# Optimization experiments

Hardware: AMD Instinct MI355X
Metric: run time of the kernel (lower is better)

## Reference

```python
import jax, jax.numpy as jnp
import numpy as np

N = 50000
E = 800000
IN_DIM = 128
HID = 128
HEADS = 8
OUT_DIM = 64
LRELU_SLOPE = 0.2


def setup_inputs() -> dict:
    key = jax.random.key(0)
    ks = jax.random.split(key, 10)
    x = jax.random.normal(ks[0], (N, IN_DIM), dtype=jnp.float32)
    edge_index = jax.random.randint(ks[1], (2, E), 0, N, dtype=jnp.int64)
    c1 = HID // HEADS  # 16
    W1 = jax.random.normal(ks[2], (IN_DIM, HID), dtype=jnp.float32) * (1.0 / np.sqrt(IN_DIM))
    as1 = jax.random.normal(ks[3], (HEADS, c1), dtype=jnp.float32) * 0.1
    ad1 = jax.random.normal(ks[4], (HEADS, c1), dtype=jnp.float32) * 0.1
    b1 = jnp.zeros((HID,), dtype=jnp.float32)
    W2 = jax.random.normal(ks[5], (HID, OUT_DIM), dtype=jnp.float32) * (1.0 / np.sqrt(HID))
    as2 = jax.random.normal(ks[6], (1, OUT_DIM), dtype=jnp.float32) * 0.1
    ad2 = jax.random.normal(ks[7], (1, OUT_DIM), dtype=jnp.float32) * 0.1
    b2 = jnp.zeros((OUT_DIM,), dtype=jnp.float32)
    return {"x": x, "edge_index": edge_index, "W1": W1, "as1": as1, "ad1": ad1,
            "b1": b1, "W2": W2, "as2": as2, "ad2": ad2, "b2": b2}


def gat_conv(x, src, dst, W, a_src, a_dst, b, heads, ch, concat):
    n = x.shape[0]
    h = (x @ W).reshape(n, heads, ch)               # [N,H,C]
    alpha_s = jnp.sum(h * a_src, axis=-1)           # [N,H]
    alpha_d = jnp.sum(h * a_dst, axis=-1)           # [N,H]
    e = jax.nn.leaky_relu(alpha_s[src] + alpha_d[dst], LRELU_SLOPE)  # [E,H]
    m = jax.ops.segment_max(e, dst, num_segments=n)  # per-dst max (self-loops guarantee nonempty)
    e = jnp.exp(e - m[dst])
    denom = jax.ops.segment_sum(e, dst, num_segments=n)
    alpha = e / (denom[dst] + 1e-16)                # [E,H]
    msg = h[src] * alpha[:, :, None]                # [E,H,C]
    out = jax.ops.segment_sum(msg, dst, num_segments=n)  # [N,H,C]
    out = out.reshape(n, heads * ch) if concat else out.mean(axis=1)
    return out + b


def reference(x, edge_index, W1, as1, ad1, b1, W2, as2, ad2, b2):
    n = x.shape[0]
    loops = jnp.arange(n, dtype=edge_index.dtype)
    src = jnp.concatenate([edge_index[0], loops])   # PyG GATConv adds self-loops
    dst = jnp.concatenate([edge_index[1], loops])
    # layer 1: GATBlock (dropout is identity at eval), heads=8, concat, ELU
    h = gat_conv(x, src, dst, W1, as1, ad1, b1, HEADS, HID // HEADS, True)
    h = jax.nn.elu(h)
    # final conv: heads=1, concat=False
    out = gat_conv(h, src, dst, W2, as2, ad2, b2, 1, OUT_DIM, False)
    return jax.nn.log_softmax(out, axis=1)
```

## Files before the change

### kernel.cpp

```cpp
#include <hip/hip_runtime.h>
#include <hip/hip_bf16.h>
#include <math.h>

#define IN_DIM 128
#define HID 128
#define HEADS 8
#define OUT_DIM 64
#define SLOPE 0.2f
#define BSHIFT 7
#define BCAP 4096
#define BCAPSHIFT 12
#define EPT 8

typedef short bf16x8 __attribute__((ext_vector_type(8)));
typedef float f32x4 __attribute__((ext_vector_type(4)));

__device__ __forceinline__ float lrelu(float x) { return fmaxf(x, SLOPE * x); }
__device__ __forceinline__ float bf2f(unsigned u) { return __uint_as_float(u << 16); }
__device__ __forceinline__ unsigned short f2bf(float f) {
    unsigned u = __float_as_uint(f);
    return (unsigned short)((u + 0x7FFF + ((u >> 16) & 1)) >> 16);
}

__global__ __launch_bounds__(256) void setup_kernel(
    const float* __restrict__ W1, const float* __restrict__ W2,
    short* __restrict__ w1t, short* __restrict__ w2t, int* __restrict__ gcursor) {
    int t = threadIdx.x;
    int b = blockIdx.x;
    if (b == 96) {
        for (int i = t; i < 512; i += 256) gcursor[i] = 0;
        return;
    }
    if (b < 64) {
        int id = b * 256 + t;
        int n = id >> 7, k = id & 127;
        w1t[id] = (short)f2bf(W1[k * 128 + n]);
    } else {
        int id = (b - 64) * 256 + t;
        int n = id >> 7, k = id & 127;
        w2t[id] = (short)f2bf(W2[k * 64 + n]);
    }
}

__device__ __forceinline__ void bscatter_body(
    int blk, int* smem, const int* __restrict__ idx,
    int* __restrict__ gcursor, unsigned* __restrict__ bucket_buf,
    int E, int N, int NB) {
    int* hist  = smem;
    int* gbase = smem + 512;
    int* lbase = smem + 1024;
    int* wtot  = smem + 1536;
    int* misc  = smem + 1540;
    unsigned* sent = (unsigned*)(smem + 1552);
    unsigned* spos = (unsigned*)(smem + 3600);
    int t = threadIdx.x;
    for (int i = t; i < 512; i += 256) hist[i] = 0;
    if (t == 0) misc[1] = 0;
    __syncthreads();
    {
        int nz = (idx[2 * t + 1] != 0) + (idx[2 * t + 513] != 0);
        if (nz) atomicAdd(&misc[1], nz);
    }
    __syncthreads();
    int flag = (misc[1] > 16) ? 1 : 0;
    int e0 = blk * (256 * EPT);
    int EN = E + N;
    unsigned ent[EPT];
    int bid[EPT];
    int loc[EPT];
#pragma unroll
    for (int k = 0; k < EPT; k++) {
        int e = e0 + k * 256 + t;
        bid[k] = -1;
        if (e < EN) {
            int src, dst;
            if (e < E) {
                if (flag) { src = idx[e]; dst = idx[E + e]; }
                else      { src = idx[2 * e]; dst = idx[2 * (E + e)]; }
            } else {
                src = dst = e - E;
            }
            int b = dst >> BSHIFT;
            bid[k] = b;
            ent[k] = ((unsigned)(dst & ((1 << BSHIFT) - 1)) << 16) | (unsigned)src;
            loc[k] = atomicAdd(&hist[b], 1);
        }
    }
    __syncthreads();
    int i0 = 2 * t;
    int a = hist[i0], b2 = hist[i0 + 1];
    int ps = a + b2;
    int lane = t & 63, w = t >> 6;
    int incl = ps;
#pragma unroll
    for (int off = 1; off < 64; off <<= 1) {
        int u = __shfl_up(incl, off, 64);
        if (lane >= off) incl += u;
    }
    if (lane == 63) wtot[w] = incl;
    __syncthreads();
    int woff = 0;
    for (int k = 0; k < w; k++) woff += wtot[k];
    int ex0 = woff + incl - ps;
    lbase[i0] = ex0;
    lbase[i0 + 1] = ex0 + a;
    if (t == 255) misc[0] = woff + incl;
    for (int i = t; i < 512; i += 256) {
        int c = hist[i];
        gbase[i] = c ? atomicAdd(&gcursor[i], c) : 0;
    }
    __syncthreads();
#pragma unroll
    for (int k = 0; k < EPT; k++) {
        if (bid[k] >= 0) {
            int p = lbase[bid[k]] + loc[k];
            int pib = gbase[bid[k]] + loc[k];
            sent[p] = ent[k];
            spos[p] = (pib < BCAP) ? (((unsigned)bid[k] << BCAPSHIFT) | (unsigned)pib)
                                   : 0xFFFFFFFFu;
        }
    }
    __syncthreads();
    int tot = misc[0];
    for (int i = t; i < tot; i += 256) {
        unsigned sp = spos[i];
        if (sp != 0xFFFFFFFFu) bucket_buf[sp] = sent[i];
    }
}

__device__ __forceinline__ void gemm1_body(
    int blk, char* smemraw, const float* __restrict__ x, const short* __restrict__ w1t,
    const float* __restrict__ a_s, const float* __restrict__ a_d,
    unsigned short* __restrict__ h1g, float* __restrict__ as_n,
    float* __restrict__ ad_n, int N) {
    short* Wt = (short*)smemraw;
    float* hT = (float*)smemraw;
    int t = threadIdx.x;
    const uint4* src = (const uint4*)w1t;
    for (int id = t; id < 128 * 16; id += 256) {
        int n = id >> 4, kg = id & 15;
        *(uint4*)&Wt[n * 128 + ((kg * 8) ^ ((n & 7) << 3))] = src[id];
    }
    __syncthreads();
    int wv = t >> 6, lane = t & 63;
    int m = lane & 15, q = lane >> 4;
    int row = blk * 64 + wv * 16 + m;
    f32x4 acc[8];
#pragma unroll
    for (int j = 0; j < 8; j++) acc[j] = (f32x4){0.f, 0.f, 0.f, 0.f};
    int msw = (m & 7) << 3;
#pragma unroll
    for (int k0 = 0; k0 < 128; k0 += 32) {
        bf16x8 a = {0, 0, 0, 0, 0, 0, 0, 0};
        if (row < N) {
            const float* xp = &x[(size_t)row * 128 + k0 + q * 8];
            float4 u0 = *(const float4*)xp;
            float4 u1 = *(const float4*)(xp + 4);
            a[0] = (short)f2bf(u0.x); a[1] = (short)f2bf(u0.y);
            a[2] = (short)f2bf(u0.z); a[3] = (short)f2bf(u0.w);
            a[4] = (short)f2bf(u1.x); a[5] = (short)f2bf(u1.y);
            a[6] = (short)f2bf(u1.z); a[7] = (short)f2bf(u1.w);
        }
#pragma unroll
        for (int j = 0; j < 8; j++) {
            bf16x8 b = *(const bf16x8*)&Wt[(j * 16 + m) * 128 + ((k0 + q * 8) ^ msw)];
            acc[j] = __builtin_amdgcn_mfma_f32_16x16x32_bf16(a, b, acc[j], 0, 0, 0);
        }
    }
    __syncthreads();
#pragma unroll
    for (int r = 0; r < 4; r++) {
        int rl = wv * 16 + q * 4 + r;
        int sw = ((rl >> 2) & 1) << 4;
        int rb = rl * 128;
#pragma unroll
        for (int j = 0; j < 8; j++)
            hT[rb + ((j * 16 + m) ^ sw)] = acc[j][r];
    }
    __syncthreads();
    int base = blk * 64;
    for (int id = t; id < 1024; id += 256) {
        int rl = id >> 4, c8 = (id & 15) * 8;
        int rg = base + rl;
        if (rg >= N) continue;
        int sw = ((rl >> 2) & 1) << 4;
        float4 u0 = *(const float4*)&hT[rl * 128 + (c8 ^ sw)];
        float4 u1 = *(const float4*)&hT[rl * 128 + ((c8 + 4) ^ sw)];
        uint4 ow;
        ow.x = (unsigned)f2bf(u0.x) | ((unsigned)f2bf(u0.y) << 16);
        ow.y = (unsigned)f2bf(u0.z) | ((unsigned)f2bf(u0.w) << 16);
        ow.z = (unsigned)f2bf(u1.x) | ((unsigned)f2bf(u1.y) << 16);
        ow.w = (unsigned)f2bf(u1.z) | ((unsigned)f2bf(u1.w) << 16);
        *(uint4*)&h1g[(size_t)rg * 128 + c8] = ow;
    }
    for (int it = t; it < 512; it += 256) {
        int rl = it >> 3, hd = it & 7;
        int rg = base + rl;
        int sw = ((rl >> 2) & 1) << 4;
        const float* ap = a_s + hd * 16;
        const float* dp = a_d + hd * 16;
        float s = 0.f, d = 0.f;
#pragma unroll
        for (int p = 0; p < 4; p++) {
            float4 u = *(const float4*)&hT[rl * 128 + ((hd * 16 + p * 4) ^ sw)];
            s += u.x * ap[p * 4] + u.y * ap[p * 4 + 1] + u.z * ap[p * 4 + 2] + u.w * ap[p * 4 + 3];
            d += u.x * dp[p * 4] + u.y * dp[p * 4 + 1] + u.z * dp[p * 4 + 2] + u.w * dp[p * 4 + 3];
        }
        if (rg < N) {
            as_n[(size_t)base * 8 + it] = s;
            ad_n[(size_t)base * 8 + it] = d;
        }
    }
}

__global__ __launch_bounds__(256) void k1_kernel(
    const int* __restrict__ idx, int* __restrict__ gcursor,
    unsigned* __restrict__ bucket_buf,
    const float* __restrict__ x, const short* __restrict__ w1t,
    const float* __restrict__ a_s, const float* __restrict__ a_d,
    unsigned short* __restrict__ h1g, float* __restrict__ as_n,
    float* __restrict__ ad_n, int E, int N, int NB, int GS) {
    __shared__ long long smem[4096];
    if ((int)blockIdx.x < GS)
        bscatter_body(blockIdx.x, (int*)smem, idx, gcursor, bucket_buf, E, N, NB);
    else
        gemm1_body(blockIdx.x - GS, (char*)smem, x, w1t, a_s, a_d, h1g, as_n, ad_n, N);
}

__device__ __forceinline__ void bsort_body(
    int b, const int* __restrict__ gcursor, const unsigned* __restrict__ bucket_buf,
    int* __restrict__ row_start, int* __restrict__ sorted_src, int N, int NB) {
    __shared__ int cnt[128];
    __shared__ int cur[128];
    __shared__ int red[4];
    __shared__ int s_w0;
    __shared__ int srt[BCAP];
    int t = threadIdx.x;
    if (t < 128) cnt[t] = 0;
    int partial = 0;
    for (int i = t; i < b; i += 256) partial += min(gcursor[i], BCAP);
#pragma unroll
    for (int msk = 32; msk > 0; msk >>= 1) partial += __shfl_xor(partial, msk, 64);
    if ((t & 63) == 0) red[t >> 6] = partial;
    __syncthreads();
    int bbase = red[0] + red[1] + red[2] + red[3];
    int c = min(gcursor[b], BCAP);
    const unsigned* buf = bucket_buf + ((size_t)b << BCAPSHIFT);
    for (int i = t; i < c; i += 256)
        atomicAdd(&cnt[(buf[i] >> 16) & 127], 1);
    __syncthreads();
    int v = (t < 128) ? cnt[t] : 0;
    int lane = t & 63;
    int incl = v;
#pragma unroll
    for (int off = 1; off < 64; off <<= 1) {
        int u = __shfl_up(incl, off, 64);
        if (lane >= off) incl += u;
    }
    if (t == 63) s_w0 = incl;
    __syncthreads();
    if (t < 128) {
        int excl = incl - v + ((t >= 64) ? s_w0 : 0);
        cur[t] = excl;
        int node = (b << BSHIFT) + t;
        if (node <= N) row_start[node] = bbase + excl;
    }
    __syncthreads();
    for (int i = t; i < c; i += 256) {
        unsigned e = buf[i];
        int lp = atomicAdd(&cur[(e >> 16) & 127], 1);
        srt[lp] = (int)(e & 0xFFFFu);
    }
    __syncthreads();
    for (int i = t; i < c; i += 256)
        sorted_src[bbase + i] = srt[i];
}

__global__ __launch_bounds__(256) void k2_kernel(
    const int* __restrict__ gcursor, const unsigned* __restrict__ bucket_buf,
    int* __restrict__ row_start, int* __restrict__ sorted_src,
    int N, int NB, int EN) {
    if (blockIdx.x == 0 && threadIdx.x < 16) sorted_src[EN + threadIdx.x] = 0;
    bsort_body(blockIdx.x, gcursor, bucket_buf, row_start, sorted_src, N, NB);
}

__global__ __launch_bounds__(256) void agg1_kernel(
    const int* __restrict__ row_start, const int* __restrict__ sorted_src,
    const float* __restrict__ as_n, const float* __restrict__ ad_n,
    const unsigned short* __restrict__ h1g, const float* __restrict__ b1,
    unsigned short* __restrict__ h1act, int N) {
    int lane = threadIdx.x & 63;
    int g = lane >> 4, j = lane & 15;
    int node = blockIdx.x * 16 + (threadIdx.x >> 6) * 4 + g;
    if (node >= N) return;
    int e4 = j >> 2;
    int hh = (j & 3) * 2;
    int hd = j >> 1;
    int hsel = hd & 1;
    int wsrc = hd >> 1;
    float2 adp = *(const float2*)&ad_n[(size_t)node * 8 + hh];
    int beg = row_start[node], end = row_start[node + 1];
    float acc[8];
#pragma unroll
    for (int k = 0; k < 8; k++) acc[k] = 0.f;
    float denom = 0.f;
    for (int i = beg; i < end; i += 4) {
        int se = sorted_src[i + e4];
        float2 asp = *(const float2*)&as_n[(size_t)se * 8 + hh];
        float w0 = __expf(lrelu(asp.x + adp.x));
        float w1 = __expf(lrelu(asp.y + adp.y));
        bool val = (i + e4 < end);
        w0 = val ? w0 : 0.f;
        w1 = val ? w1 : 0.f;
#pragma unroll
        for (int e = 0; e < 4; e++) {
            int sl = e * 4 + wsrc;
            int sg = __shfl(se, sl, 16);
            float wa = __shfl(w0, sl, 16);
            float wb = __shfl(w1, sl, 16);
            float wv = hsel ? wb : wa;
            uint4 hv = *(const uint4*)&h1g[(size_t)sg * 128 + j * 8];
            acc[0] += wv * bf2f(hv.x & 0xffffu);
            acc[1] += wv * bf2f(hv.x >> 16);
            acc[2] += wv * bf2f(hv.y & 0xffffu);
            acc[3] += wv * bf2f(hv.y >> 16);
            acc[4] += wv * bf2f(hv.z & 0xffffu);
            acc[5] += wv * bf2f(hv.z >> 16);
            acc[6] += wv * bf2f(hv.w & 0xffffu);
            acc[7] += wv * bf2f(hv.w >> 16);
            denom += wv;
        }
    }
    float inv = 1.f / (denom + 1e-16f);
    int c0 = j * 8;
    unsigned ow[4];
#pragma unroll
    for (int p = 0; p < 4; p++) {
        float v0 = acc[2 * p] * inv + b1[c0 + 2 * p];
        float v1 = acc[2 * p + 1] * inv + b1[c0 + 2 * p + 1];
        v0 = (v0 > 0.f) ? v0 : (__expf(v0) - 1.f);
        v1 = (v1 > 0.f) ? v1 : (__expf(v1) - 1.f);
        ow[p] = (unsigned)f2bf(v0) | ((unsigned)f2bf(v1) << 16);
    }
    *(uint4*)&h1act[(size_t)node * 128 + c0] = make_uint4(ow[0], ow[1], ow[2], ow[3]);
}

__global__ __launch_bounds__(256) void gemm2_kernel(
    const unsigned short* __restrict__ h1act, const short* __restrict__ w2t,
    const float* __restrict__ a_s, const float* __restrict__ a_d,
    unsigned short* __restrict__ h2g, float* __restrict__ as_n,
    float* __restrict__ ad_n, int N) {
    __shared__ short Wt[64 * 136];
    int t = threadIdx.x;
    const uint4* src = (const uint4*)w2t;
    for (int id = t; id < 64 * 16; id += 256) {
        int n = id >> 4, kg = id & 15;
        *(uint4*)&Wt[n * 136 + kg * 8] = src[id];
    }
    __syncthreads();
    int wv = t >> 6, lane = t & 63;
    int m = lane & 15, q = lane >> 4;
    int row = blockIdx.x * 64 + wv * 16 + m;
    f32x4 acc[4];
#pragma unroll
    for (int j = 0; j < 4; j++) acc[j] = (f32x4){0.f, 0.f, 0.f, 0.f};
#pragma unroll
    for (int k0 = 0; k0 < 128; k0 += 32) {
        bf16x8 a = {0, 0, 0, 0, 0, 0, 0, 0};
        if (row < N) a = *(const bf16x8*)&h1act[(size_t)row * 128 + k0 + q * 8];
#pragma unroll
        for (int j = 0; j < 4; j++) {
            bf16x8 b = *(const bf16x8*)&Wt[(j * 16 + m) * 136 + k0 + q * 8];
            acc[j] = __builtin_amdgcn_mfma_f32_16x16x32_bf16(a, b, acc[j], 0, 0, 0);
        }
    }
    float asl[4], adl[4];
#pragma unroll
    for (int j = 0; j < 4; j++) { asl[j] = a_s[j * 16 + m]; adl[j] = a_d[j * 16 + m]; }
    int rbase = blockIdx.x * 64 + wv * 16 + q * 4;
#pragma unroll
    for (int r = 0; r < 4; r++) {
        int rr = rbase + r;
        float s = 0.f, d = 0.f;
#pragma unroll
        for (int j = 0; j < 4; j++) {
            s += acc[j][r] * asl[j];
            d += acc[j][r] * adl[j];
        }
#pragma unroll
        for (int msk = 8; msk > 0; msk >>= 1) {
            s += __shfl_xor(s, msk, 64);
            d += __shfl_xor(d, msk, 64);
        }
        if (rr < N) {
            if (m == 0) { as_n[rr] = s; ad_n[rr] = d; }
#pragma unroll
            for (int j = 0; j < 4; j++)
                h2g[(size_t)rr * 64 + j * 16 + m] = f2bf(acc[j][r]);
        }
    }
}

__global__ __launch_bounds__(256) void agg2_kernel(
    const int* __restrict__ row_start, const int* __restrict__ sorted_src,
    const float* __restrict__ as_n, const float* __restrict__ ad_n,
    const unsigned short* __restrict__ h2g, const float* __restrict__ b2,
    float* __restrict__ out, int N) {
    int lane = threadIdx.x & 63;
    int g = lane >> 4, j = lane & 15;
    int node = blockIdx.x * 16 + (threadIdx.x >> 6) * 4 + g;
    if (node >= N) return;
    int e4 = j >> 2;
    float adv = ad_n[node];
    int beg = row_start[node], end = row_start[node + 1];
    float acc[4];
#pragma unroll
    for (int k = 0; k < 4; k++) acc[k] = 0.f;
    float denom = 0.f;
    for (int i = beg; i < end; i += 4) {
        int se = sorted_src[i + e4];
        float w = __expf(lrelu(as_n[se] + adv));
        w = (i + e4 < end) ? w : 0.f;
#pragma unroll
        for (int e = 0; e < 4; e++) {
            int sg = __shfl(se, e * 4, 16);
            float wvv = __shfl(w, e * 4, 16);
            uint2 hv = *(const uint2*)&h2g[(size_t)sg * 64 + j * 4];
            acc[0] += wvv * bf2f(hv.x & 0xffffu);
            acc[1] += wvv * bf2f(hv.x >> 16);
            acc[2] += wvv * bf2f(hv.y & 0xffffu);
            acc[3] += wvv * bf2f(hv.y >> 16);
            denom += wvv;
        }
    }
    float inv = 1.f / (denom + 1e-16f);
    int c0 = j * 4;
    float v[4];
#pragma unroll
    for (int k = 0; k < 4; k++) v[k] = acc[k] * inv + b2[c0 + k];
    float mx = fmaxf(fmaxf(v[0], v[1]), fmaxf(v[2], v[3]));
#pragma unroll
    for (int msk = 8; msk > 0; msk >>= 1) mx = fmaxf(mx, __shfl_xor(mx, msk, 64));
    float ex = __expf(v[0] - mx) + __expf(v[1] - mx) + __expf(v[2] - mx) + __expf(v[3] - mx);
#pragma unroll
    for (int msk = 8; msk > 0; msk >>= 1) ex += __shfl_xor(ex, msk, 64);
    float lse = mx + __logf(ex);
    *(float4*)&out[(size_t)node * 64 + c0] = make_float4(v[0] - lse, v[1] - lse, v[2] - lse, v[3] - lse);
}

extern "C" void kernel_launch(void* const* d_in, const int* in_sizes, int n_in,
                              void* d_out, int out_size, void* d_ws, size_t ws_size,
                              hipStream_t stream) {
    const float* x   = (const float*)d_in[0];
    const int*   idx = (const int*)d_in[1];
    const float* W1  = (const float*)d_in[2];
    const float* as1 = (const float*)d_in[3];
    const float* ad1 = (const float*)d_in[4];
    const float* b1  = (const float*)d_in[5];
    const float* W2  = (const float*)d_in[6];
    const float* as2 = (const float*)d_in[7];
    const float* ad2 = (const float*)d_in[8];
    const float* b2  = (const float*)d_in[9];
    float* out = (float*)d_out;

    const int N = in_sizes[0] / IN_DIM;
    const int E = in_sizes[1] / 2;
    const int EN = E + N;
    const int NB = (N + (1 << BSHIFT) - 1) >> BSHIFT;
    const int GS = (EN + 256 * EPT - 1) / (256 * EPT);
    const int T1 = (N + 63) / 64;

    unsigned short* h1g   = (unsigned short*)d_ws;
    unsigned short* h1act = h1g + (size_t)N * 128;
    unsigned short* h2g   = h1act + (size_t)N * 128;
    float* as1n = (float*)(h2g + (size_t)N * 64);
    float* ad1n = as1n + (size_t)N * 8;
    float* as2n = ad1n + (size_t)N * 8;
    float* ad2n = as2n + (size_t)N;
    int* row_start  = (int*)(ad2n + (size_t)N);
    int* gcursor    = row_start + N + 1;
    unsigned* bucket_buf = (unsigned*)(gcursor + 512);
    int* sorted_src = (int*)(bucket_buf + ((size_t)NB << BCAPSHIFT));
    short* w1t = (short*)((((uintptr_t)(sorted_src + EN + 16)) + 15) & ~(uintptr_t)15);
    short* w2t = w1t + 128 * 128;
    (void)ws_size; (void)n_in; (void)out_size;

    setup_kernel<<<97, 256, 0, stream>>>(W1, W2, w1t, w2t, gcursor);
    k1_kernel<<<GS + T1, 256, 0, stream>>>(idx, gcursor, bucket_buf,
                                           x, w1t, as1, ad1, h1g, as1n, ad1n, E, N, NB, GS);
    k2_kernel<<<NB, 256, 0, stream>>>(gcursor, bucket_buf, row_start, sorted_src, N, NB, EN);
    agg1_kernel<<<(N + 15) / 16, 256, 0, stream>>>(row_start, sorted_src, as1n, ad1n, h1g, b1, h1act, N);
    gemm2_kernel<<<T1, 256, 0, stream>>>(h1act, w2t, as2, ad2, h2g, as2n, ad2n, N);
    agg2_kernel<<<(N + 15) / 16, 256, 0, stream>>>(row_start, sorted_src, as2n, ad2n, h2g, b2, out, N);
}
```

Before: 187.8 us.

## Fuse layer-1 aggregation with layer-2 GEMM via shared-memory tile

Merges the layer-1 attention aggregation and the layer-2 MFMA projection into one kernel. Each block aggregates 64 nodes, writes the ELU-activated bf16 rows into a swizzled LDS tile, then runs the 64x128x64 MFMA GEMM from LDS. This removes the h1act global write and re-read plus one launch. In exchange, blocks are 4x fewer (64 nodes each, processed serially in 4 passes) and use about 33KB of LDS, which can reduce occupancy and the latency hiding available to the gather-bound aggregation.

```diff
diff --git a/kernel.cpp b/kernel.cpp
--- a/kernel.cpp
+++ b/kernel.cpp
@@ -284,108 +284,112 @@
     bsort_body(blockIdx.x, gcursor, bucket_buf, row_start, sorted_src, N, NB);
 }
 
-__global__ __launch_bounds__(256) void agg1_kernel(
+__global__ __launch_bounds__(256) void mid_kernel(
     const int* __restrict__ row_start, const int* __restrict__ sorted_src,
     const float* __restrict__ as_n, const float* __restrict__ ad_n,
     const unsigned short* __restrict__ h1g, const float* __restrict__ b1,
-    unsigned short* __restrict__ h1act, int N) {
-    int lane = threadIdx.x & 63;
+    const short* __restrict__ w2t, const float* __restrict__ a_s2,
+    const float* __restrict__ a_d2, unsigned short* __restrict__ h2g,
+    float* __restrict__ as2n, float* __restrict__ ad2n, int N) {
+    __shared__ short hA[64 * 128];
+    __shared__ short Wt[64 * 136];
+    int t = threadIdx.x;
+    const uint4* srcw = (const uint4*)w2t;
+    for (int id = t; id < 64 * 16; id += 256) {
+        int n = id >> 4, kg = id & 15;
+        *(uint4*)&Wt[n * 136 + kg * 8] = srcw[id];
+    }
+    int lane = t & 63;
     int g = lane >> 4, j = lane & 15;
-    int node = blockIdx.x * 16 + (threadIdx.x >> 6) * 4 + g;
-    if (node >= N) return;
+    int base = blockIdx.x * 64;
+    int grp16 = (t >> 6) * 4 + g;
     int e4 = j >> 2;
     int hh = (j & 3) * 2;
     int hd = j >> 1;
     int hsel = hd & 1;
     int wsrc = hd >> 1;
-    float2 adp = *(const float2*)&ad_n[(size_t)node * 8 + hh];
-    int beg = row_start[node], end = row_start[node + 1];
-    float acc[8];
-#pragma unroll
-    for (int k = 0; k < 8; k++) acc[k] = 0.f;
-    float denom = 0.f;
-    for (int i = beg; i < end; i += 4) {
-        int se = sorted_src[i + e4];
-        float2 asp = *(const float2*)&as_n[(size_t)se * 8 + hh];
-        float w0 = __expf(lrelu(asp.x + adp.x));
-        float w1 = __expf(lrelu(asp.y + adp.y));
-        bool val = (i + e4 < end);
-        w0 = val ? w0 : 0.f;
-        w1 = val ? w1 : 0.f;
-#pragma unroll
-        for (int e = 0; e < 4; e++) {
-            int sl = e * 4 + wsrc;
-            int sg = __shfl(se, sl, 16);
-            float wa = __shfl(w0, sl, 16);
-            float wb = __shfl(w1, sl, 16);
-            float wv = hsel ? wb : wa;
-            uint4 hv = *(const uint4*)&h1g[(size_t)sg * 128 + j * 8];
-            acc[0] += wv * bf2f(hv.x & 0xffffu);
-            acc[1] += wv * bf2f(hv.x >> 16);
-            acc[2] += wv * bf2f(hv.y & 0xffffu);
-            acc[3] += wv * bf2f(hv.y >> 16);
-            acc[4] += wv * bf2f(hv.z & 0xffffu);
-            acc[5] += wv * bf2f(hv.z >> 16);
-            acc[6] += wv * bf2f(hv.w & 0xffffu);
-            acc[7] += wv * bf2f(hv.w >> 16);
-            denom += wv;
-        }
-    }
-    float inv = 1.f / (denom + 1e-16f);
-    int c0 = j * 8;
-    unsigned ow[4];
-#pragma unroll
-    for (int p = 0; p < 4; p++) {
-        float v0 = acc[2 * p] * inv + b1[c0 + 2 * p];
-        float v1 = acc[2 * p + 1] * inv + b1[c0 + 2 * p + 1];
-        v0 = (v0 > 0.f) ? v0 : (__expf(v0) - 1.f);
-        v1 = (v1 > 0.f) ? v1 : (__expf(v1) - 1.f);
-        ow[p] = (unsigned)f2bf(v0) | ((unsigned)f2bf(v1) << 16);
-    }
-    *(uint4*)&h1act[(size_t)node * 128 + c0] = make_uint4(ow[0], ow[1], ow[2], ow[3]);
-}
-
-__global__ __launch_bounds__(256) void gemm2_kernel(
-    const unsigned short* __restrict__ h1act, const short* __restrict__ w2t,
-    const float* __restrict__ a_s, const float* __restrict__ a_d,
-    unsigned short* __restrict__ h2g, float* __restrict__ as_n,
-    float* __restrict__ ad_n, int N) {
-    __shared__ short Wt[64 * 136];
-    int t = threadIdx.x;
-    const uint4* src = (const uint4*)w2t;
-    for (int id = t; id < 64 * 16; id += 256) {
-        int n = id >> 4, kg = id & 15;
-        *(uint4*)&Wt[n * 136 + kg * 8] = src[id];
-    }
-    __syncthreads();
-    int wv = t >> 6, lane = t & 63;
+    for (int ni = 0; ni < 4; ni++) {
+        int rowl = ni * 16 + grp16;
+        int node = base + rowl;
+        float acc[8];
+#pragma unroll
+        for (int k = 0; k < 8; k++) acc[k] = 0.f;
+        float denom = 0.f;
+        if (node < N) {
+            float2 adp = *(const float2*)&ad_n[(size_t)node * 8 + hh];
+            int beg = row_start[node], end = row_start[node + 1];
+            for (int i = beg; i < end; i += 4) {
+                int se = sorted_src[i + e4];
+                float2 asp = *(const float2*)&as_n[(size_t)se * 8 + hh];
+                float w0 = __expf(lrelu(asp.x + adp.x));
+                float w1 = __expf(lrelu(asp.y + adp.y));
+                bool val = (i + e4 < end);
+                w0 = val ? w0 : 0.f;
+                w1 = val ? w1 : 0.f;
+#pragma unroll
+                for (int e = 0; e < 4; e++) {
+                    int sl = e * 4 + wsrc;
+                    int sg = __shfl(se, sl, 16);
+                    float wa = __shfl(w0, sl, 16);
+                    float wb = __shfl(w1, sl, 16);
+                    float wv = hsel ? wb : wa;
+                    uint4 hv = *(const uint4*)&h1g[(size_t)sg * 128 + j * 8];
+                    acc[0] += wv * bf2f(hv.x & 0xffffu);
+                    acc[1] += wv * bf2f(hv.x >> 16);
+                    acc[2] += wv * bf2f(hv.y & 0xffffu);
+                    acc[3] += wv * bf2f(hv.y >> 16);
+                    acc[4] += wv * bf2f(hv.z & 0xffffu);
+                    acc[5] += wv * bf2f(hv.z >> 16);
+                    acc[6] += wv * bf2f(hv.w & 0xffffu);
+                    acc[7] += wv * bf2f(hv.w >> 16);
+                    denom += wv;
+                }
+            }
+        }
+        float inv = 1.f / (denom + 1e-16f);
+        int c0 = j * 8;
+        unsigned ow[4];
+#pragma unroll
+        for (int p = 0; p < 4; p++) {
+            float v0 = acc[2 * p] * inv + b1[c0 + 2 * p];
+            float v1 = acc[2 * p + 1] * inv + b1[c0 + 2 * p + 1];
+            v0 = (v0 > 0.f) ? v0 : (__expf(v0) - 1.f);
+            v1 = (v1 > 0.f) ? v1 : (__expf(v1) - 1.f);
+            ow[p] = (unsigned)f2bf(v0) | ((unsigned)f2bf(v1) << 16);
+        }
+        uint4 val = (node < N) ? make_uint4(ow[0], ow[1], ow[2], ow[3])
+                               : make_uint4(0, 0, 0, 0);
+        *(uint4*)&hA[rowl * 128 + ((j * 8) ^ ((rowl & 7) << 3))] = val;
+    }
+    __syncthreads();
+    int wv = t >> 6;
     int m = lane & 15, q = lane >> 4;
-    int row = blockIdx.x * 64 + wv * 16 + m;
-    f32x4 acc[4];
-#pragma unroll
-    for (int j = 0; j < 4; j++) acc[j] = (f32x4){0.f, 0.f, 0.f, 0.f};
+    int rowl = wv * 16 + m;
+    int rsw = (rowl & 7) << 3;
+    f32x4 acc2[4];
+#pragma unroll
+    for (int j4 = 0; j4 < 4; j4++) acc2[j4] = (f32x4){0.f, 0.f, 0.f, 0.f};
 #pragma unroll
     for (int k0 = 0; k0 < 128; k0 += 32) {
-        bf16x8 a = {0, 0, 0, 0, 0, 0, 0, 0};
-        if (row < N) a = *(const bf16x8*)&h1act[(size_t)row * 128 + k0 + q * 8];
-#pragma unroll
-        for (int j = 0; j < 4; j++) {
-            bf16x8 b = *(const bf16x8*)&Wt[(j * 16 + m) * 136 + k0 + q * 8];
-            acc[j] = __builtin_amdgcn_mfma_f32_16x16x32_bf16(a, b, acc[j], 0, 0, 0);
+        bf16x8 a = *(const bf16x8*)&hA[rowl * 128 + ((k0 + q * 8) ^ rsw)];
+#pragma unroll
+        for (int j4 = 0; j4 < 4; j4++) {
+            bf16x8 b = *(const bf16x8*)&Wt[(j4 * 16 + m) * 136 + k0 + q * 8];
+            acc2[j4] = __builtin_amdgcn_mfma_f32_16x16x32_bf16(a, b, acc2[j4], 0, 0, 0);
         }
     }
     float asl[4], adl[4];
 #pragma unroll
-    for (int j = 0; j < 4; j++) { asl[j] = a_s[j * 16 + m]; adl[j] = a_d[j * 16 + m]; }
-    int rbase = blockIdx.x * 64 + wv * 16 + q * 4;
+    for (int j4 = 0; j4 < 4; j4++) { asl[j4] = a_s2[j4 * 16 + m]; adl[j4] = a_d2[j4 * 16 + m]; }
+    int rbase = base + wv * 16 + q * 4;
 #pragma unroll
     for (int r = 0; r < 4; r++) {
         int rr = rbase + r;
         float s = 0.f, d = 0.f;
 #pragma unroll
-        for (int j = 0; j < 4; j++) {
-            s += acc[j][r] * asl[j];
-            d += acc[j][r] * adl[j];
+        for (int j4 = 0; j4 < 4; j4++) {
+            s += acc2[j4][r] * asl[j4];
+            d += acc2[j4][r] * adl[j4];
         }
 #pragma unroll
         for (int msk = 8; msk > 0; msk >>= 1) {
@@ -393,10 +397,10 @@
             d += __shfl_xor(d, msk, 64);
         }
         if (rr < N) {
-            if (m == 0) { as_n[rr] = s; ad_n[rr] = d; }
-#pragma unroll
-            for (int j = 0; j < 4; j++)
-                h2g[(size_t)rr * 64 + j * 16 + m] = f2bf(acc[j][r]);
+            if (m == 0) { as2n[rr] = s; ad2n[rr] = d; }
+#pragma unroll
+            for (int j4 = 0; j4 < 4; j4++)
+                h2g[(size_t)rr * 64 + j4 * 16 + m] = f2bf(acc2[j4][r]);
         }
     }
 }
@@ -489,7 +493,7 @@
     k1_kernel<<<GS + T1, 256, 0, stream>>>(idx, gcursor, bucket_buf,
                                            x, w1t, as1, ad1, h1g, as1n, ad1n, E, N, NB, GS);
     k2_kernel<<<NB, 256, 0, stream>>>(gcursor, bucket_buf, row_start, sorted_src, N, NB, EN);
-    agg1_kernel<<<(N + 15) / 16, 256, 0, stream>>>(row_start, sorted_src, as1n, ad1n, h1g, b1, h1act, N);
-    gemm2_kernel<<<T1, 256, 0, stream>>>(h1act, w2t, as2, ad2, h2g, as2n, ad2n, N);
+    mid_kernel<<<T1, 256, 0, stream>>>(row_start, sorted_src, as1n, ad1n, h1g, b1,
+                                       w2t, as2, ad2, h2g, as2n, ad2n, N);
     agg2_kernel<<<(N + 15) / 16, 256, 0, stream>>>(row_start, sorted_src, as2n, ad2n, h2g, b2, out, N);
 }
```

After: 184.5 us. Within noise of the previous version (-1.7%).
